# Kernel optimization log

Measured on AMD Instinct MI355X. Metric: run time of the kernel, lower is better.

The kernel has to match this reference:

```python
import jax, jax.numpy as jnp
import numpy as np

EMB = 512
HEADS = 8

def setup_inputs() -> dict:
    key = jax.random.key(0)
    ks = jax.random.split(key, 9)
    s = 1.0 / np.sqrt(EMB)
    return {
        'x':  jax.random.normal(ks[0], (4, 2048, EMB), dtype=jnp.float32),
        'Wq': jax.random.uniform(ks[1], (EMB, EMB), jnp.float32, -s, s),
        'bq': jax.random.uniform(ks[2], (EMB,), jnp.float32, -s, s),
        'Wk': jax.random.uniform(ks[3], (EMB, EMB), jnp.float32, -s, s),
        'bk': jax.random.uniform(ks[4], (EMB,), jnp.float32, -s, s),
        'Wv': jax.random.uniform(ks[5], (EMB, EMB), jnp.float32, -s, s),
        'bv': jax.random.uniform(ks[6], (EMB,), jnp.float32, -s, s),
        'Wo': jax.random.uniform(ks[7], (EMB, EMB), jnp.float32, -s, s),
        'bo': jax.random.uniform(ks[8], (EMB,), jnp.float32, -s, s),
    }

def reference(x, Wq, bq, Wk, bk, Wv, bv, Wo, bo):
    b, n, e = x.shape
    h = HEADS
    d = e // h
    def split_heads(t):
        return t.reshape(b, n, h, d).transpose(0, 2, 1, 3)  # b h n d
    q = split_heads(x @ Wq.T + bq)
    k = split_heads(x @ Wk.T + bk)
    v = split_heads(x @ Wv.T + bv)
    energy = jnp.einsum('bhqd,bhkd->bhqk', q, k)
    scaling = jnp.sqrt(jnp.float32(e))  # NOTE: sqrt(emb_size), not sqrt(head_dim), per source
    att = jax.nn.softmax(energy / scaling, axis=-1)
    out = jnp.einsum('bhal,bhlv->bhav', att, v)  # b h n d
    out = out.transpose(0, 2, 1, 3).reshape(b, n, e)
    return out @ Wo.T + bo
```

## Files before the change

### kernel.cpp

```cpp
#include <hip/hip_runtime.h>

typedef float f32x4 __attribute__((ext_vector_type(4)));
typedef float f32x16 __attribute__((ext_vector_type(16)));
typedef short bf16x8 __attribute__((ext_vector_type(8)));
typedef unsigned int uint;
typedef unsigned short ushort_t;

#define EMB    512
#define NSEQ   2048
#define NBATCH 4
#define NHEAD  8
#define MROWS  (NBATCH * NSEQ)
#define CEXP   0.06375872f

__device__ __forceinline__ uint f2bf(float x) {
    uint u = __builtin_bit_cast(uint, x);
    return (u + 0x7fffu + ((u >> 16) & 1u)) >> 16;
}

__global__ __launch_bounds__(256)
void prep(const float* __restrict__ x,
          const float* __restrict__ Wq, const float* __restrict__ Wk,
          const float* __restrict__ Wv, const float* __restrict__ Wo,
          const float* __restrict__ bq, const float* __restrict__ bk,
          const float* __restrict__ bv,
          ushort_t* __restrict__ xb, ushort_t* __restrict__ Wqkvb,
          float* __restrict__ bqkv, ushort_t* __restrict__ Wob) {
    int t = blockIdx.x * 256 + threadIdx.x;
    {
        float4 v = ((const float4*)x)[t];
        uint2 p;
        p.x = f2bf(v.x) | (f2bf(v.y) << 16);
        p.y = f2bf(v.z) | (f2bf(v.w) << 16);
        ((uint2*)xb)[t] = p;
    }
    if (t < 65536) {
        float4 a = ((const float4*)Wq)[t];
        float4 b = ((const float4*)Wk)[t];
        float4 c = ((const float4*)Wv)[t];
        float4 d = ((const float4*)Wo)[t];
        uint2 p;
        p.x = f2bf(a.x) | (f2bf(a.y) << 16); p.y = f2bf(a.z) | (f2bf(a.w) << 16);
        ((uint2*)Wqkvb)[t] = p;
        p.x = f2bf(b.x) | (f2bf(b.y) << 16); p.y = f2bf(b.z) | (f2bf(b.w) << 16);
        ((uint2*)Wqkvb)[t + 65536] = p;
        p.x = f2bf(c.x) | (f2bf(c.y) << 16); p.y = f2bf(c.z) | (f2bf(c.w) << 16);
        ((uint2*)Wqkvb)[t + 131072] = p;
        p.x = f2bf(d.x) | (f2bf(d.y) << 16); p.y = f2bf(d.z) | (f2bf(d.w) << 16);
        ((uint2*)Wob)[t] = p;
    }
    if (t < 512) {
        bqkv[t] = bq[t]; bqkv[512 + t] = bk[t]; bqkv[1024 + t] = bv[t];
    }
}

template<int MODE>
__global__ __launch_bounds__(256)
void gemm128(const ushort_t* __restrict__ A, const ushort_t* __restrict__ BT,
             const float* __restrict__ bias, ushort_t* __restrict__ oQK,
             ushort_t* __restrict__ oVT, float* __restrict__ oC) {
    __shared__ ushort_t As[128][40];
    __shared__ ushort_t Bs[128][40];
    __shared__ float ep[32][132];
    const int tid = threadIdx.x, wave = tid >> 6, lane = tid & 63;
    const int m0 = blockIdx.x * 128, n0 = blockIdx.y * 128;
    const int wr = (wave & 1) * 64, wc = (wave >> 1) * 64;

    f32x4 acc[4][4];
#pragma unroll
    for (int i = 0; i < 4; ++i)
#pragma unroll
        for (int j = 0; j < 4; ++j) acc[i][j] = (f32x4){0.f, 0.f, 0.f, 0.f};

    const int sr = tid >> 1, sh = (tid & 1) * 16;
    const ushort_t* Arow = A + (size_t)(m0 + sr) * 512 + sh;
    const ushort_t* Brow = BT + (size_t)(n0 + sr) * 512 + sh;
    const int fr = lane & 15, fc = (lane >> 4) * 8;

    for (int kt = 0; kt < 16; ++kt) {
        uint4 a0 = *(const uint4*)(Arow + kt * 32);
        uint4 a1 = *(const uint4*)(Arow + kt * 32 + 8);
        uint4 b0 = *(const uint4*)(Brow + kt * 32);
        uint4 b1 = *(const uint4*)(Brow + kt * 32 + 8);
        __syncthreads();
        *(uint4*)&As[sr][sh] = a0;  *(uint4*)&As[sr][sh + 8] = a1;
        *(uint4*)&Bs[sr][sh] = b0;  *(uint4*)&Bs[sr][sh + 8] = b1;
        __syncthreads();
        bf16x8 af[4], bf[4];
#pragma unroll
        for (int i = 0; i < 4; ++i) af[i] = *(const bf16x8*)&As[wr + i * 16 + fr][fc];
#pragma unroll
        for (int j = 0; j < 4; ++j) bf[j] = *(const bf16x8*)&Bs[wc + j * 16 + fr][fc];
#pragma unroll
        for (int i = 0; i < 4; ++i)
#pragma unroll
            for (int j = 0; j < 4; ++j)
                acc[i][j] = __builtin_amdgcn_mfma_f32_16x16x32_bf16(af[i], bf[j], acc[i][j], 0, 0, 0);
    }

    const int col_l = lane & 15, row_l = (lane >> 4) * 4;

    if (MODE == 0 && n0 >= 1024) {
#pragma unroll
        for (int j = 0; j < 4; ++j) {
            const int col = n0 + wc + j * 16 + col_l;
            const float bv = bias[col];
#pragma unroll
            for (int i = 0; i < 4; ++i) {
                const int row = m0 + wr + i * 16 + row_l;
                f32x4 v = acc[i][j];
                v += (f32x4){bv, bv, bv, bv};
                const int e = col - 1024;
                const int b = row >> 11, tok = row & 2047;
                uint2 p;
                p.x = f2bf(v[0]) | (f2bf(v[1]) << 16);
                p.y = f2bf(v[2]) | (f2bf(v[3]) << 16);
                *(uint2*)&oVT[((size_t)(b * 512 + e)) * 2048 + tok] = p;
            }
        }
        return;
    }

    const float scale = (MODE == 0 && n0 < 512) ? CEXP : 1.0f;
    float bv[4];
#pragma unroll
    for (int j = 0; j < 4; ++j) bv[j] = bias[n0 + wc + j * 16 + col_l];

    const int erow = tid >> 3, eseg = (tid & 7) * 16;
#pragma unroll
    for (int c = 0; c < 4; ++c) {
        __syncthreads();
        if (wr == (c >> 1) * 64) {
#pragma unroll
            for (int ii = 0; ii < 2; ++ii) {
                const int i = (c & 1) * 2 + ii;
#pragma unroll
                for (int j = 0; j < 4; ++j) {
                    f32x4 v = acc[i][j];
#pragma unroll
                    for (int r = 0; r < 4; ++r)
                        ep[ii * 16 + row_l + r][wc + j * 16 + col_l] = (v[r] + bv[j]) * scale;
                }
            }
        }
        __syncthreads();
        const int grow = m0 + c * 32 + erow;
        if (MODE == 0) {
            uint4 o0, o1;
#pragma unroll
            for (int k = 0; k < 4; ++k) {
                uint lo = f2bf(ep[erow][eseg + k * 2])     | (f2bf(ep[erow][eseg + k * 2 + 1]) << 16);
                uint hi = f2bf(ep[erow][eseg + 8 + k * 2]) | (f2bf(ep[erow][eseg + 9 + k * 2]) << 16);
                ((uint*)&o0)[k] = lo; ((uint*)&o1)[k] = hi;
            }
            *(uint4*)&oQK[(size_t)grow * 1024 + n0 + eseg]     = o0;
            *(uint4*)&oQK[(size_t)grow * 1024 + n0 + eseg + 8] = o1;
        } else {
#pragma unroll
            for (int k = 0; k < 4; ++k) {
                f32x4 v = *(const f32x4*)&ep[erow][eseg + k * 4];
                *(f32x4*)&oC[(size_t)grow * 512 + n0 + eseg + k * 4] = v;
            }
        }
    }
}

template<int NSLICE>
__global__ __launch_bounds__(256)
void attn_mfma(const ushort_t* __restrict__ QK, const ushort_t* __restrict__ VT,
               float* __restrict__ Op, float* __restrict__ Lp,
               ushort_t* __restrict__ AO) {
    __shared__ ushort_t Ks[64][72];
    __shared__ ushort_t Vs[64][72];
    __shared__ ushort_t Ps[4][32][72];
    __shared__ float ls[128];

    const int tid = threadIdx.x, w = tid >> 6, lane = tid & 63;
    const int qt = blockIdx.x, bh = blockIdx.y, b = bh >> 3, h = bh & 7;
    const int slice = (NSLICE > 1) ? blockIdx.z : 0;
    const int l31 = lane & 31, lhi = lane >> 5;

    const size_t qrow = (size_t)(b * NSEQ + qt * 128 + w * 32 + l31);
    bf16x8 qf[4];
#pragma unroll
    for (int ks = 0; ks < 4; ++ks)
        qf[ks] = *(const bf16x8*)&QK[qrow * 1024 + h * 64 + ks * 16 + lhi * 8];

    f32x16 accO[2];
#pragma unroll
    for (int i = 0; i < 16; ++i) { accO[0][i] = 0.f; accO[1][i] = 0.f; }
    float lpart = 0.f;

    const int sr = tid & 63, sc = (tid >> 6) * 16;
    const ushort_t* Kg = QK + (size_t)(b * NSEQ) * 1024 + 512 + h * 64;
    const ushort_t* Vg = VT + ((size_t)(b * 512 + h * 64)) * 2048;

    const int kt0 = slice * (32 / NSLICE), kt1 = kt0 + 32 / NSLICE;
    for (int kt = kt0; kt < kt1; ++kt) {
        const int k0 = kt * 64;
        uint4 kv0 = *(const uint4*)&Kg[(size_t)(k0 + sr) * 1024 + sc];
        uint4 kv1 = *(const uint4*)&Kg[(size_t)(k0 + sr) * 1024 + sc + 8];
        uint4 vv0 = *(const uint4*)&Vg[(size_t)sr * 2048 + k0 + sc];
        uint4 vv1 = *(const uint4*)&Vg[(size_t)sr * 2048 + k0 + sc + 8];
        __syncthreads();
        *(uint4*)&Ks[sr][sc] = kv0;  *(uint4*)&Ks[sr][sc + 8] = kv1;
        *(uint4*)&Vs[sr][sc] = vv0;  *(uint4*)&Vs[sr][sc + 8] = vv1;
        __syncthreads();

        f32x16 st[2];
#pragma unroll
        for (int i = 0; i < 16; ++i) { st[0][i] = 0.f; st[1][i] = 0.f; }
#pragma unroll
        for (int ks = 0; ks < 4; ++ks) {
            bf16x8 ka0 = *(const bf16x8*)&Ks[l31][ks * 16 + lhi * 8];
            bf16x8 ka1 = *(const bf16x8*)&Ks[32 + l31][ks * 16 + lhi * 8];
            st[0] = __builtin_amdgcn_mfma_f32_32x32x16_bf16(ka0, qf[ks], st[0], 0, 0, 0);
            st[1] = __builtin_amdgcn_mfma_f32_32x32x16_bf16(ka1, qf[ks], st[1], 0, 0, 0);
        }

#pragma unroll
        for (int ms = 0; ms < 2; ++ms) {
#pragma unroll
            for (int g = 0; g < 4; ++g) {
                uint u0 = __builtin_bit_cast(uint, __builtin_amdgcn_exp2f(st[ms][g * 4 + 0]));
                uint u1 = __builtin_bit_cast(uint, __builtin_amdgcn_exp2f(st[ms][g * 4 + 1]));
                uint u2 = __builtin_bit_cast(uint, __builtin_amdgcn_exp2f(st[ms][g * 4 + 2]));
                uint u3 = __builtin_bit_cast(uint, __builtin_amdgcn_exp2f(st[ms][g * 4 + 3]));
                lpart += __builtin_bit_cast(float, u0 & 0xffff0000u)
                       + __builtin_bit_cast(float, u1 & 0xffff0000u)
                       + __builtin_bit_cast(float, u2 & 0xffff0000u)
                       + __builtin_bit_cast(float, u3 & 0xffff0000u);
                uint2 p;
                p.x = (u0 >> 16) | (u1 & 0xffff0000u);
                p.y = (u2 >> 16) | (u3 & 0xffff0000u);
                *(uint2*)&Ps[w][l31][ms * 32 + g * 8 + lhi * 4] = p;
            }
        }

#pragma unroll
        for (int ks = 0; ks < 4; ++ks) {
            bf16x8 pa  = *(const bf16x8*)&Ps[w][l31][ks * 16 + lhi * 8];
            bf16x8 vb0 = *(const bf16x8*)&Vs[l31][ks * 16 + lhi * 8];
            bf16x8 vb1 = *(const bf16x8*)&Vs[32 + l31][ks * 16 + lhi * 8];
            accO[0] = __builtin_amdgcn_mfma_f32_32x32x16_bf16(pa, vb0, accO[0], 0, 0, 0);
            accO[1] = __builtin_amdgcn_mfma_f32_32x32x16_bf16(pa, vb1, accO[1], 0, 0, 0);
        }
    }

    float lfull = lpart + __shfl_xor(lpart, 32);

    if (NSLICE == 1) {
        if (lane < 32) ls[w * 32 + l31] = lfull;
        __syncthreads();
#pragma unroll
        for (int g = 0; g < 4; ++g) {
            float4 lv = *(const float4*)&ls[w * 32 + g * 8 + lhi * 4];
#pragma unroll
            for (int r = 0; r < 4; ++r) {
                const float inv = 1.0f / ((const float*)&lv)[r];
                const int rowp = g * 8 + lhi * 4 + r;
                const size_t orow = (size_t)(b * NSEQ + qt * 128 + w * 32 + rowp);
                AO[orow * 512 + h * 64 + l31]      = (ushort_t)f2bf(accO[0][g * 4 + r] * inv);
                AO[orow * 512 + h * 64 + 32 + l31] = (ushort_t)f2bf(accO[1][g * 4 + r] * inv);
            }
        }
    } else {
        const size_t rowbase = (size_t)(b * NSEQ + qt * 128 + w * 32);
        if (lane < 32) Lp[(size_t)slice * 65536 + (rowbase + l31) * 8 + h] = lfull;
        float* Os = Op + (size_t)slice * 4194304;
#pragma unroll
        for (int g = 0; g < 4; ++g) {
#pragma unroll
            for (int r = 0; r < 4; ++r) {
                const int rowp = g * 8 + lhi * 4 + r;
                const size_t orow = rowbase + rowp;
                Os[orow * 512 + h * 64 + l31]      = accO[0][g * 4 + r];
                Os[orow * 512 + h * 64 + 32 + l31] = accO[1][g * 4 + r];
            }
        }
    }
}

__global__ __launch_bounds__(256)
void combine2(const float* __restrict__ Op, const float* __restrict__ Lp,
              ushort_t* __restrict__ AO) {
    const int t = blockIdx.x * 256 + threadIdx.x;
    const int row = t >> 7;
    const int c4  = (t & 127) * 4;
    const int h = c4 >> 6;
    float4 a = ((const float4*)Op)[t];
    float4 b = ((const float4*)(Op + 4194304))[t];
    const float inv = 1.0f / (Lp[row * 8 + h] + Lp[65536 + row * 8 + h]);
    uint2 p;
    p.x = f2bf((a.x + b.x) * inv) | (f2bf((a.y + b.y) * inv) << 16);
    p.y = f2bf((a.z + b.z) * inv) | (f2bf((a.w + b.w) * inv) << 16);
    ((uint2*)AO)[t] = p;
}

extern "C" void kernel_launch(void* const* d_in, const int* in_sizes, int n_in,
                              void* d_out, int out_size, void* d_ws, size_t ws_size,
                              hipStream_t stream) {
    const float* x  = (const float*)d_in[0];
    const float* Wq = (const float*)d_in[1];
    const float* bq = (const float*)d_in[2];
    const float* Wk = (const float*)d_in[3];
    const float* bk = (const float*)d_in[4];
    const float* Wv = (const float*)d_in[5];
    const float* bv = (const float*)d_in[6];
    const float* Wo = (const float*)d_in[7];
    const float* bo = (const float*)d_in[8];

    char* ws = (char*)d_ws;
    ushort_t* xb    = (ushort_t*)(ws);
    ushort_t* Wqkvb = (ushort_t*)(ws + 8388608);
    ushort_t* Wob   = (ushort_t*)(ws + 9961472);
    float*    bqkv  = (float*)   (ws + 10485760);
    ushort_t* QKb   = (ushort_t*)(ws + 10491904);
    ushort_t* VTg   = (ushort_t*)(ws + 27269120);
    ushort_t* AOb   = (ushort_t*)(ws + 35657728);
    float*    Opart = (float*)   (ws + 44046336);
    float*    Lpart = (float*)   (ws + 77600768);
    const bool split = ws_size >= 78125056;

    prep<<<4096, 256, 0, stream>>>(x, Wq, Wk, Wv, Wo, bq, bk, bv,
                                   xb, Wqkvb, bqkv, Wob);
    gemm128<0><<<dim3(64, 12), 256, 0, stream>>>(xb, Wqkvb, bqkv, QKb, VTg, nullptr);
    if (split) {
        attn_mfma<2><<<dim3(16, 32, 2), 256, 0, stream>>>(QKb, VTg, Opart, Lpart, nullptr);
        combine2<<<4096, 256, 0, stream>>>(Opart, Lpart, AOb);
    } else {
        attn_mfma<1><<<dim3(16, 32), 256, 0, stream>>>(QKb, VTg, nullptr, nullptr, AOb);
    }
    gemm128<1><<<dim3(64, 4), 256, 0, stream>>>(AOb, Wob, bo, nullptr, nullptr, (float*)d_out);
}
```

Baseline: 194.9 us.

## Keep P in registers via lane shuffles, shrink attention blocks, use direct-to-LDS GEMM loads

The attention kernel now builds the P operand for the PV MFMA in registers. It exchanges half-rows across lanes with shfl_xor and swaps operand roles, instead of staging P through shared memory. Blocks are reduced to 128 threads with 64 query rows, doubling the grid, and the partial output is written token-major so a new tiled combine kernel transposes it back through LDS. The GEMM tile loads switch to global_load_lds, which skips register staging, but the LDS row padding is removed and that may introduce bank conflicts.

```diff
diff --git a/kernel.cpp b/kernel.cpp
--- a/kernel.cpp
+++ b/kernel.cpp
@@ -16,6 +16,12 @@
 __device__ __forceinline__ uint f2bf(float x) {
     uint u = __builtin_bit_cast(uint, x);
     return (u + 0x7fffu + ((u >> 16) & 1u)) >> 16;
+}
+
+__device__ __forceinline__ void glds16(const void* g, void* l) {
+    __builtin_amdgcn_global_load_lds(
+        (const __attribute__((address_space(1))) uint*)g,
+        (__attribute__((address_space(3))) uint*)l, 16, 0, 0);
 }
 
 __global__ __launch_bounds__(256)
@@ -59,8 +65,8 @@
 void gemm128(const ushort_t* __restrict__ A, const ushort_t* __restrict__ BT,
              const float* __restrict__ bias, ushort_t* __restrict__ oQK,
              ushort_t* __restrict__ oVT, float* __restrict__ oC) {
-    __shared__ ushort_t As[128][40];
-    __shared__ ushort_t Bs[128][40];
+    __shared__ ushort_t As[128][32];
+    __shared__ ushort_t Bs[128][32];
     __shared__ float ep[32][132];
     const int tid = threadIdx.x, wave = tid >> 6, lane = tid & 63;
     const int m0 = blockIdx.x * 128, n0 = blockIdx.y * 128;
@@ -72,19 +78,22 @@
 #pragma unroll
         for (int j = 0; j < 4; ++j) acc[i][j] = (f32x4){0.f, 0.f, 0.f, 0.f};
 
-    const int sr = tid >> 1, sh = (tid & 1) * 16;
-    const ushort_t* Arow = A + (size_t)(m0 + sr) * 512 + sh;
-    const ushort_t* Brow = BT + (size_t)(n0 + sr) * 512 + sh;
+    const int grow = wave * 16 + (lane >> 2);
+    const int gcol = (lane & 3) * 8;
+    const ushort_t* Ag = A  + (size_t)(m0 + grow) * 512 + gcol;
+    const ushort_t* Bg = BT + (size_t)(n0 + grow) * 512 + gcol;
+    ushort_t* lA0 = &As[wave * 16][0];
+    ushort_t* lA1 = &As[64 + wave * 16][0];
+    ushort_t* lB0 = &Bs[wave * 16][0];
+    ushort_t* lB1 = &Bs[64 + wave * 16][0];
     const int fr = lane & 15, fc = (lane >> 4) * 8;
 
     for (int kt = 0; kt < 16; ++kt) {
-        uint4 a0 = *(const uint4*)(Arow + kt * 32);
-        uint4 a1 = *(const uint4*)(Arow + kt * 32 + 8);
-        uint4 b0 = *(const uint4*)(Brow + kt * 32);
-        uint4 b1 = *(const uint4*)(Brow + kt * 32 + 8);
-        __syncthreads();
-        *(uint4*)&As[sr][sh] = a0;  *(uint4*)&As[sr][sh + 8] = a1;
-        *(uint4*)&Bs[sr][sh] = b0;  *(uint4*)&Bs[sr][sh + 8] = b1;
+        __syncthreads();
+        glds16(Ag + kt * 32,             lA0);
+        glds16(Ag + kt * 32 + 64 * 512,  lA1);
+        glds16(Bg + kt * 32,             lB0);
+        glds16(Bg + kt * 32 + 64 * 512,  lB1);
         __syncthreads();
         bf16x8 af[4], bf[4];
 #pragma unroll
@@ -144,7 +153,7 @@
             }
         }
         __syncthreads();
-        const int grow = m0 + c * 32 + erow;
+        const int grow2 = m0 + c * 32 + erow;
         if (MODE == 0) {
             uint4 o0, o1;
 #pragma unroll
@@ -153,34 +162,33 @@
                 uint hi = f2bf(ep[erow][eseg + 8 + k * 2]) | (f2bf(ep[erow][eseg + 9 + k * 2]) << 16);
                 ((uint*)&o0)[k] = lo; ((uint*)&o1)[k] = hi;
             }
-            *(uint4*)&oQK[(size_t)grow * 1024 + n0 + eseg]     = o0;
-            *(uint4*)&oQK[(size_t)grow * 1024 + n0 + eseg + 8] = o1;
+            *(uint4*)&oQK[(size_t)grow2 * 1024 + n0 + eseg]     = o0;
+            *(uint4*)&oQK[(size_t)grow2 * 1024 + n0 + eseg + 8] = o1;
         } else {
 #pragma unroll
             for (int k = 0; k < 4; ++k) {
                 f32x4 v = *(const f32x4*)&ep[erow][eseg + k * 4];
-                *(f32x4*)&oC[(size_t)grow * 512 + n0 + eseg + k * 4] = v;
+                *(f32x4*)&oC[(size_t)grow2 * 512 + n0 + eseg + k * 4] = v;
             }
         }
     }
 }
 
 template<int NSLICE>
-__global__ __launch_bounds__(256)
+__global__ __launch_bounds__(128)
 void attn_mfma(const ushort_t* __restrict__ QK, const ushort_t* __restrict__ VT,
                float* __restrict__ Op, float* __restrict__ Lp,
                ushort_t* __restrict__ AO) {
     __shared__ ushort_t Ks[64][72];
     __shared__ ushort_t Vs[64][72];
-    __shared__ ushort_t Ps[4][32][72];
-    __shared__ float ls[128];
 
     const int tid = threadIdx.x, w = tid >> 6, lane = tid & 63;
     const int qt = blockIdx.x, bh = blockIdx.y, b = bh >> 3, h = bh & 7;
     const int slice = (NSLICE > 1) ? blockIdx.z : 0;
     const int l31 = lane & 31, lhi = lane >> 5;
 
-    const size_t qrow = (size_t)(b * NSEQ + qt * 128 + w * 32 + l31);
+    const int tok = qt * 64 + w * 32 + l31;
+    const size_t qrow = (size_t)(b * NSEQ + tok);
     bf16x8 qf[4];
 #pragma unroll
     for (int ks = 0; ks < 4; ++ks)
@@ -191,110 +199,122 @@
     for (int i = 0; i < 16; ++i) { accO[0][i] = 0.f; accO[1][i] = 0.f; }
     float lpart = 0.f;
 
-    const int sr = tid & 63, sc = (tid >> 6) * 16;
+    const int sr = tid & 63, sc = (tid >> 6) * 32;
     const ushort_t* Kg = QK + (size_t)(b * NSEQ) * 1024 + 512 + h * 64;
     const ushort_t* Vg = VT + ((size_t)(b * 512 + h * 64)) * 2048;
 
     const int kt0 = slice * (32 / NSLICE), kt1 = kt0 + 32 / NSLICE;
     for (int kt = kt0; kt < kt1; ++kt) {
         const int k0 = kt * 64;
-        uint4 kv0 = *(const uint4*)&Kg[(size_t)(k0 + sr) * 1024 + sc];
-        uint4 kv1 = *(const uint4*)&Kg[(size_t)(k0 + sr) * 1024 + sc + 8];
-        uint4 vv0 = *(const uint4*)&Vg[(size_t)sr * 2048 + k0 + sc];
-        uint4 vv1 = *(const uint4*)&Vg[(size_t)sr * 2048 + k0 + sc + 8];
-        __syncthreads();
-        *(uint4*)&Ks[sr][sc] = kv0;  *(uint4*)&Ks[sr][sc + 8] = kv1;
-        *(uint4*)&Vs[sr][sc] = vv0;  *(uint4*)&Vs[sr][sc + 8] = vv1;
-        __syncthreads();
-
-        f32x16 st[2];
-#pragma unroll
-        for (int i = 0; i < 16; ++i) { st[0][i] = 0.f; st[1][i] = 0.f; }
-#pragma unroll
-        for (int ks = 0; ks < 4; ++ks) {
-            bf16x8 ka0 = *(const bf16x8*)&Ks[l31][ks * 16 + lhi * 8];
-            bf16x8 ka1 = *(const bf16x8*)&Ks[32 + l31][ks * 16 + lhi * 8];
-            st[0] = __builtin_amdgcn_mfma_f32_32x32x16_bf16(ka0, qf[ks], st[0], 0, 0, 0);
-            st[1] = __builtin_amdgcn_mfma_f32_32x32x16_bf16(ka1, qf[ks], st[1], 0, 0, 0);
-        }
+        uint4 kv[4], vv[4];
+#pragma unroll
+        for (int k = 0; k < 4; ++k) {
+            kv[k] = *(const uint4*)&Kg[(size_t)(k0 + sr) * 1024 + sc + 8 * k];
+            vv[k] = *(const uint4*)&Vg[(size_t)sr * 2048 + k0 + sc + 8 * k];
+        }
+        __syncthreads();
+#pragma unroll
+        for (int k = 0; k < 4; ++k) {
+            *(uint4*)&Ks[sr][sc + 8 * k] = kv[k];
+            *(uint4*)&Vs[sr][sc + 8 * k] = vv[k];
+        }
+        __syncthreads();
 
 #pragma unroll
         for (int ms = 0; ms < 2; ++ms) {
-#pragma unroll
-            for (int g = 0; g < 4; ++g) {
-                uint u0 = __builtin_bit_cast(uint, __builtin_amdgcn_exp2f(st[ms][g * 4 + 0]));
-                uint u1 = __builtin_bit_cast(uint, __builtin_amdgcn_exp2f(st[ms][g * 4 + 1]));
-                uint u2 = __builtin_bit_cast(uint, __builtin_amdgcn_exp2f(st[ms][g * 4 + 2]));
-                uint u3 = __builtin_bit_cast(uint, __builtin_amdgcn_exp2f(st[ms][g * 4 + 3]));
-                lpart += __builtin_bit_cast(float, u0 & 0xffff0000u)
-                       + __builtin_bit_cast(float, u1 & 0xffff0000u)
-                       + __builtin_bit_cast(float, u2 & 0xffff0000u)
-                       + __builtin_bit_cast(float, u3 & 0xffff0000u);
-                uint2 p;
-                p.x = (u0 >> 16) | (u1 & 0xffff0000u);
-                p.y = (u2 >> 16) | (u3 & 0xffff0000u);
-                *(uint2*)&Ps[w][l31][ms * 32 + g * 8 + lhi * 4] = p;
-            }
-        }
-
-#pragma unroll
-        for (int ks = 0; ks < 4; ++ks) {
-            bf16x8 pa  = *(const bf16x8*)&Ps[w][l31][ks * 16 + lhi * 8];
-            bf16x8 vb0 = *(const bf16x8*)&Vs[l31][ks * 16 + lhi * 8];
-            bf16x8 vb1 = *(const bf16x8*)&Vs[32 + l31][ks * 16 + lhi * 8];
-            accO[0] = __builtin_amdgcn_mfma_f32_32x32x16_bf16(pa, vb0, accO[0], 0, 0, 0);
-            accO[1] = __builtin_amdgcn_mfma_f32_32x32x16_bf16(pa, vb1, accO[1], 0, 0, 0);
-        }
-    }
-
-    float lfull = lpart + __shfl_xor(lpart, 32);
+            f32x16 st;
+#pragma unroll
+            for (int i = 0; i < 16; ++i) st[i] = 0.f;
+#pragma unroll
+            for (int ks = 0; ks < 4; ++ks) {
+                bf16x8 ka = *(const bf16x8*)&Ks[ms * 32 + l31][ks * 16 + lhi * 8];
+                st = __builtin_amdgcn_mfma_f32_32x32x16_bf16(ka, qf[ks], st, 0, 0, 0);
+            }
+            uint dd[8], ee[8];
+#pragma unroll
+            for (int i = 0; i < 8; ++i) {
+                uint ua = __builtin_bit_cast(uint, __builtin_amdgcn_exp2f(st[2 * i]));
+                uint ub = __builtin_bit_cast(uint, __builtin_amdgcn_exp2f(st[2 * i + 1]));
+                lpart += __builtin_bit_cast(float, ua & 0xffff0000u)
+                       + __builtin_bit_cast(float, ub & 0xffff0000u);
+                dd[i] = (ua >> 16) | (ub & 0xffff0000u);
+            }
+#pragma unroll
+            for (int i = 0; i < 8; ++i) ee[i] = (uint)__shfl_xor((int)dd[i], 32);
+#pragma unroll
+            for (int s = 0; s < 2; ++s) {
+                union { uint u[4]; bf16x8 v; } B;
+                B.u[0] = lhi ? ee[4 * s + 2] : dd[4 * s + 0];
+                B.u[1] = lhi ? ee[4 * s + 3] : dd[4 * s + 1];
+                B.u[2] = lhi ? dd[4 * s + 2] : ee[4 * s + 0];
+                B.u[3] = lhi ? dd[4 * s + 3] : ee[4 * s + 1];
+                const int step = ms * 2 + s;
+                bf16x8 va0 = *(const bf16x8*)&Vs[l31][step * 16 + lhi * 8];
+                bf16x8 va1 = *(const bf16x8*)&Vs[32 + l31][step * 16 + lhi * 8];
+                accO[0] = __builtin_amdgcn_mfma_f32_32x32x16_bf16(va0, B.v, accO[0], 0, 0, 0);
+                accO[1] = __builtin_amdgcn_mfma_f32_32x32x16_bf16(va1, B.v, accO[1], 0, 0, 0);
+            }
+        }
+    }
+
+    const float lfull = lpart + __shfl_xor(lpart, 32);
 
     if (NSLICE == 1) {
-        if (lane < 32) ls[w * 32 + l31] = lfull;
-        __syncthreads();
-#pragma unroll
-        for (int g = 0; g < 4; ++g) {
-            float4 lv = *(const float4*)&ls[w * 32 + g * 8 + lhi * 4];
-#pragma unroll
-            for (int r = 0; r < 4; ++r) {
-                const float inv = 1.0f / ((const float*)&lv)[r];
-                const int rowp = g * 8 + lhi * 4 + r;
-                const size_t orow = (size_t)(b * NSEQ + qt * 128 + w * 32 + rowp);
-                AO[orow * 512 + h * 64 + l31]      = (ushort_t)f2bf(accO[0][g * 4 + r] * inv);
-                AO[orow * 512 + h * 64 + 32 + l31] = (ushort_t)f2bf(accO[1][g * 4 + r] * inv);
-            }
-        }
+        const float inv = 1.0f / lfull;
+#pragma unroll
+        for (int hf = 0; hf < 2; ++hf)
+#pragma unroll
+            for (int r = 0; r < 16; ++r) {
+                const int d = (r & 3) + 8 * (r >> 2) + 4 * lhi + 32 * hf;
+                AO[((size_t)(b * NSEQ + tok)) * 512 + h * 64 + d] =
+                    (ushort_t)f2bf(accO[hf][r] * inv);
+            }
     } else {
-        const size_t rowbase = (size_t)(b * NSEQ + qt * 128 + w * 32);
-        if (lane < 32) Lp[(size_t)slice * 65536 + (rowbase + l31) * 8 + h] = lfull;
+        if (lane < 32) Lp[(size_t)slice * 65536 + bh * 2048 + tok] = lfull;
         float* Os = Op + (size_t)slice * 4194304;
 #pragma unroll
-        for (int g = 0; g < 4; ++g) {
-#pragma unroll
-            for (int r = 0; r < 4; ++r) {
-                const int rowp = g * 8 + lhi * 4 + r;
-                const size_t orow = rowbase + rowp;
-                Os[orow * 512 + h * 64 + l31]      = accO[0][g * 4 + r];
-                Os[orow * 512 + h * 64 + 32 + l31] = accO[1][g * 4 + r];
-            }
-        }
+        for (int hf = 0; hf < 2; ++hf)
+#pragma unroll
+            for (int r = 0; r < 16; ++r) {
+                const int d = (r & 3) + 8 * (r >> 2) + 4 * lhi + 32 * hf;
+                Os[((size_t)(bh * 64 + d)) * 2048 + tok] = accO[hf][r];
+            }
     }
 }
 
 __global__ __launch_bounds__(256)
-void combine2(const float* __restrict__ Op, const float* __restrict__ Lp,
-              ushort_t* __restrict__ AO) {
-    const int t = blockIdx.x * 256 + threadIdx.x;
-    const int row = t >> 7;
-    const int c4  = (t & 127) * 4;
-    const int h = c4 >> 6;
-    float4 a = ((const float4*)Op)[t];
-    float4 b = ((const float4*)(Op + 4194304))[t];
-    const float inv = 1.0f / (Lp[row * 8 + h] + Lp[65536 + row * 8 + h]);
-    uint2 p;
-    p.x = f2bf((a.x + b.x) * inv) | (f2bf((a.y + b.y) * inv) << 16);
-    p.y = f2bf((a.z + b.z) * inv) | (f2bf((a.w + b.w) * inv) << 16);
-    ((uint2*)AO)[t] = p;
+void combine2T(const float* __restrict__ Op, const float* __restrict__ Lp,
+               ushort_t* __restrict__ AO) {
+    __shared__ float T[64][68];
+    const int tid = threadIdx.x;
+    const int tc = blockIdx.x, bh = blockIdx.y;
+    const int b = bh >> 3, h = bh & 7;
+    const int tok0 = tc * 64;
+
+    const int d = tid >> 2, ts = (tid & 3) * 16;
+    const float* P0 = Op + ((size_t)(bh * 64 + d)) * 2048 + tok0 + ts;
+    const float* P1 = P0 + 4194304;
+#pragma unroll
+    for (int k = 0; k < 4; ++k) {
+        f32x4 a = *(const f32x4*)(P0 + 4 * k);
+        f32x4 c = *(const f32x4*)(P1 + 4 * k);
+        *(f32x4*)&T[d][ts + 4 * k] = a + c;
+    }
+    __syncthreads();
+
+    const int tk = tid >> 2, ds = (tid & 3) * 16;
+    const int tok = tok0 + tk;
+    const float inv = 1.0f / (Lp[bh * 2048 + tok] + Lp[65536 + bh * 2048 + tok]);
+    uint o[8];
+#pragma unroll
+    for (int k = 0; k < 8; ++k) {
+        float a = T[ds + 2 * k][tk] * inv;
+        float c = T[ds + 2 * k + 1][tk] * inv;
+        o[k] = f2bf(a) | (f2bf(c) << 16);
+    }
+    ushort_t* dst = AO + ((size_t)(b * NSEQ + tok)) * 512 + h * 64 + ds;
+    *(uint4*)dst       = *(const uint4*)&o[0];
+    *(uint4*)(dst + 8) = *(const uint4*)&o[4];
 }
 
 extern "C" void kernel_launch(void* const* d_in, const int* in_sizes, int n_in,
@@ -326,10 +346,10 @@
                                    xb, Wqkvb, bqkv, Wob);
     gemm128<0><<<dim3(64, 12), 256, 0, stream>>>(xb, Wqkvb, bqkv, QKb, VTg, nullptr);
     if (split) {
-        attn_mfma<2><<<dim3(16, 32, 2), 256, 0, stream>>>(QKb, VTg, Opart, Lpart, nullptr);
-        combine2<<<4096, 256, 0, stream>>>(Opart, Lpart, AOb);
+        attn_mfma<2><<<dim3(32, 32, 2), 128, 0, stream>>>(QKb, VTg, Opart, Lpart, nullptr);
+        combine2T<<<dim3(32, 32), 256, 0, stream>>>(Opart, Lpart, AOb);
     } else {
-        attn_mfma<1><<<dim3(16, 32), 256, 0, stream>>>(QKb, VTg, nullptr, nullptr, AOb);
+        attn_mfma<1><<<dim3(32, 32, 1), 128, 0, stream>>>(QKb, VTg, nullptr, nullptr, AOb);
     }
     gemm128<1><<<dim3(64, 4), 256, 0, stream>>>(AOb, Wob, bo, nullptr, nullptr, (float*)d_out);
 }
```

Measured after the change: 369.3 us. 1.9x slower.
